# Performance work log

Measured on AMD Instinct MI355X. Metric: run time of the kernel, lower is better.

The kernel has to match this reference:

```python
import jax, jax.numpy as jnp
from jax import lax
import numpy as np

H = 256      # encoder_hidden
F = 256      # variance predictor filter_size
K = 3        # kernel_size
NBINS = 256  # variance_embedding n_bins
B, S, T = 64, 512, 2048


def conv1d(x, w, b, pad):
    # x: [B, L, Cin], w: [K, Cin, Cout] -> [B, L, Cout]
    y = lax.conv_general_dilated(x, w, window_strides=(1,), padding=[(pad, pad)],
                                 dimension_numbers=('NWC', 'WIO', 'NWC'))
    return y + b


def layer_norm(x, g, b, eps=1e-5):
    mu = jnp.mean(x, -1, keepdims=True)
    v = jnp.mean((x - mu) ** 2, -1, keepdims=True)
    return (x - mu) * lax.rsqrt(v + eps) * g + b


def predictor(x, mask, w1, b1, g1, be1, w2, b2, g2, be2, lw, lb):
    h = jax.nn.relu(conv1d(x, w1, b1, (K - 1) // 2))
    h = layer_norm(h, g1, be1)
    h = jax.nn.relu(conv1d(h, w2, b2, 1))  # padding=1 hardcoded in original conv1d_2
    h = layer_norm(h, g2, be2)
    out = (h @ lw + lb)[..., 0]            # [B, L]
    return jnp.where(mask, 0.0, out)       # masked_fill(mask, 0.0)


def setup_inputs():
    key = jax.random.key(0)
    ks = jax.random.split(key, 16)
    inp = {
        'x': jax.random.normal(ks[0], (B, S, H), jnp.float32),
        'pitch_target': jax.random.normal(ks[1], (B, S), jnp.float32),
        'energy_target': jax.random.normal(ks[2], (B, S), jnp.float32),
        'src_mask': jnp.zeros((B, S), bool),
        'duration': jax.random.randint(ks[3], (B, S), 0, 4, jnp.int32),
        'max_len': T,
    }
    i = 4
    for p in ['d', 'p', 'e']:
        inp[p + '_w1'] = jax.random.normal(ks[i], (K, H, F), jnp.float32) * 0.05; i += 1
        inp[p + '_b1'] = jnp.zeros((F,), jnp.float32)
        inp[p + '_g1'] = jnp.ones((F,), jnp.float32)
        inp[p + '_be1'] = jnp.zeros((F,), jnp.float32)
        inp[p + '_w2'] = jax.random.normal(ks[i], (K, F, F), jnp.float32) * 0.05; i += 1
        inp[p + '_b2'] = jnp.zeros((F,), jnp.float32)
        inp[p + '_g2'] = jnp.ones((F,), jnp.float32)
        inp[p + '_be2'] = jnp.zeros((F,), jnp.float32)
        inp[p + '_lw'] = jax.random.normal(ks[i], (F, 1), jnp.float32) * 0.05; i += 1
        inp[p + '_lb'] = jnp.zeros((1,), jnp.float32)
    inp['p_table'] = jax.random.normal(ks[i], (NBINS, H), jnp.float32) * 0.02; i += 1
    inp['e_table'] = jax.random.normal(ks[i], (NBINS, H), jnp.float32) * 0.02
    return inp


def reference(x, pitch_target, energy_target, src_mask, duration, max_len,
              d_w1, d_b1, d_g1, d_be1, d_w2, d_b2, d_g2, d_be2, d_lw, d_lb,
              p_w1, p_b1, p_g1, p_be1, p_w2, p_b2, p_g2, p_be2, p_lw, p_lb,
              e_w1, e_b1, e_g1, e_be1, e_w2, e_b2, e_g2, e_be2, e_lw, e_lb,
              p_table, e_table):
    # linear-quantized bins over the data range (stats.json min/max -> [-2, 2] for randn data)
    bins = jnp.linspace(-2.0, 2.0, NBINS - 1, dtype=jnp.float32)

    log_d_pred = predictor(x, src_mask, d_w1, d_b1, d_g1, d_be1, d_w2, d_b2, d_g2, d_be2, d_lw, d_lb)

    # phoneme-level pitch (training path: target given -> embed bucketized target)
    p_pred = predictor(x, src_mask, p_w1, p_b1, p_g1, p_be1, p_w2, p_b2, p_g2, p_be2, p_lw, p_lb)
    p_emb = p_table[jnp.searchsorted(bins, pitch_target, side='left')]  # torch.bucketize(right=False)
    x = x + p_emb

    # phoneme-level energy (predictor runs on x AFTER pitch embedding, as in original)
    e_pred = predictor(x, src_mask, e_w1, e_b1, e_g1, e_be1, e_w2, e_b2, e_g2, e_be2, e_lw, e_lb)
    e_emb = e_table[jnp.searchsorted(bins, energy_target, side='left')]
    x = x + e_emb

    # Length regulation: expand phoneme i duration[b, i] times, pad to max_len.
    cum = jnp.cumsum(duration, axis=1)                 # [B, S]
    mel_len = cum[:, -1]                               # [B]
    frames = jnp.arange(max_len)                       # [T]
    # frame t maps to first phoneme i with cum[i] > t
    idx = jax.vmap(lambda c: jnp.searchsorted(c, frames, side='right'))(cum)  # [B, T]
    idx = jnp.minimum(idx, duration.shape[1] - 1)
    mel = jnp.take_along_axis(x, idx[:, :, None], axis=1)                     # [B, T, H]
    valid = frames[None, :] < mel_len[:, None]
    mel = jnp.where(valid[:, :, None], mel, 0.0)       # zero-pad beyond mel_len

    d_rounded = duration
    return (mel, p_pred, e_pred, log_d_pred, d_rounded, mel_len)
```

## Files before the change

### kernel.cpp

```cpp
#include <hip/hip_runtime.h>
#include <cstdint>
#include <cstddef>


#define HH 256
#define SS 512
#define BB 64
#define TT 2048
#define LSTR 264

typedef __bf16 bf16;
typedef __attribute__((ext_vector_type(8))) __bf16 bf16x8;
typedef __attribute__((ext_vector_type(4))) __bf16 bf16x4;
typedef __attribute__((ext_vector_type(4))) float f32x4;

static constexpr size_t WSZ  = (size_t)3 * HH * HH;
static constexpr size_t H1SZ = (size_t)BB * SS * HH;

__device__ __forceinline__ float edge_val(int j) {
    const float step = 4.0f / 254.0f;
    if (j == 254) return 2.0f;
    return __fadd_rn(-2.0f, __fmul_rn((float)j, step));
}
__device__ __forceinline__ int bucket256(float v) {
    int lo = 0, hi = 255;
    while (lo < hi) {
        int mid = (lo + hi) >> 1;
        if (edge_val(mid) < v) lo = mid + 1; else hi = mid;
    }
    return lo;
}

__global__ __launch_bounds__(256) void prep_kernel(
    const float* __restrict__ w0, const float* __restrict__ w1,
    const float* __restrict__ w2, const float* __restrict__ w3,
    const float* __restrict__ w4, const float* __restrict__ w5,
    bf16* __restrict__ wp,
    const int* __restrict__ dur, int* __restrict__ idxb, int* __restrict__ mli,
    float* __restrict__ drnd, float* __restrict__ mlen,
    const float* __restrict__ x, const float* __restrict__ pt,
    const float* __restrict__ ptab,
    bf16* __restrict__ x1, bf16* __restrict__ x2)
{
    const int tid = threadIdx.x;
    if (blockIdx.x < 18) {
        const int cv = blockIdx.x / 3, k = blockIdx.x % 3;
        const float* wsel[6] = {w0, w1, w2, w3, w4, w5};
        const float* wk = wsel[cv] + (size_t)k * HH * HH;
        bf16* o = wp + ((size_t)(cv * 3 + k)) * HH * HH;
        for (int fb = 0; fb < 16; ++fb) {
            #pragma unroll
            for (int h = 0; h < 2; ++h) {
                const int idx  = tid + 256 * h;
                const int kcb  = idx >> 6, lane = idx & 63;
                const int f    = fb * 16 + (lane & 15);
                const int c0   = kcb * 32 + (lane >> 4) * 8;
                bf16x8 v;
                #pragma unroll
                for (int j = 0; j < 8; ++j) v[j] = (bf16)wk[(size_t)(c0 + j) * HH + f];
                *(bf16x8*)(o + (((size_t)fb * 8 + kcb) * 64 + lane) * 8) = v;
            }
        }
    } else if (blockIdx.x < 82) {
        __shared__ int sb[SS];
        const int b = blockIdx.x - 18;
        const int d0 = dur[b * SS + tid];
        const int d1 = dur[b * SS + tid + 256];
        drnd[b * SS + tid]       = (float)d0;
        drnd[b * SS + tid + 256] = (float)d1;
        sb[tid]       = d0;
        sb[tid + 256] = d1;
        __syncthreads();
        for (int off = 1; off < SS; off <<= 1) {
            const int a0 = (tid >= off) ? sb[tid - off] : 0;
            const int a1 = (tid + 256 >= off) ? sb[tid + 256 - off] : 0;
            __syncthreads();
            sb[tid] += a0;
            sb[tid + 256] += a1;
            __syncthreads();
        }
        {
            const int hi = sb[tid], lo = hi - d0;
            for (int j = lo; j < hi; ++j) idxb[b * TT + j] = tid;
        }
        {
            const int hi = sb[tid + 256], lo = hi - d1;
            for (int j = lo; j < hi; ++j) idxb[b * TT + j] = tid + 256;
        }
        if (tid == 255) { mlen[b] = (float)sb[SS - 1]; mli[b] = sb[SS - 1]; }
    } else {
        const int row = (blockIdx.x - 82) * 8 + (tid >> 5);
        const int c   = (tid & 31) * 8;
        const int pb  = bucket256(pt[row]);
        const float4 v0 = *(const float4*)(x + (size_t)row * HH + c);
        const float4 v1 = *(const float4*)(x + (size_t)row * HH + c + 4);
        const float4 t0 = *(const float4*)(ptab + (size_t)pb * HH + c);
        const float4 t1 = *(const float4*)(ptab + (size_t)pb * HH + c + 4);
        bf16x8 a, b2;
        a[0] = (bf16)v0.x; a[1] = (bf16)v0.y; a[2] = (bf16)v0.z; a[3] = (bf16)v0.w;
        a[4] = (bf16)v1.x; a[5] = (bf16)v1.y; a[6] = (bf16)v1.z; a[7] = (bf16)v1.w;
        b2[0] = (bf16)(v0.x + t0.x); b2[1] = (bf16)(v0.y + t0.y);
        b2[2] = (bf16)(v0.z + t0.z); b2[3] = (bf16)(v0.w + t0.w);
        b2[4] = (bf16)(v1.x + t1.x); b2[5] = (bf16)(v1.y + t1.y);
        b2[6] = (bf16)(v1.z + t1.z); b2[7] = (bf16)(v1.w + t1.w);
        *(bf16x8*)(x1 + (size_t)row * HH + c) = a;
        *(bf16x8*)(x2 + (size_t)row * HH + c) = b2;
    }
}

struct Args3 {
    const float* bias[3];
    const float* g[3];
    const float* be[3];
    const float* lw[3];
    const float* lb[3];
    float*       out[3];
};

__global__ __launch_bounds__(256, 3) void conv_fused(
    const bf16* __restrict__ x1,
    const bf16* __restrict__ x2,
    const bf16* __restrict__ wpk,
    Args3 a1, Args3 a2,
    const uint8_t* __restrict__ mask)
{
    __shared__ alignas(16) bf16 tile[82 * LSTR];
    __shared__ float red_s[80][4], red_q[80][4];
    __shared__ float ln_m[80], ln_r[80];

    const int tid    = threadIdx.x;
    const int pred   = blockIdx.x >> 9;
    const int within = blockIdx.x & 511;
    const int b      = within >> 3;
    const int s0     = (within & 7) * 64;

    const int lane = tid & 63;
    const int wv   = tid >> 6;

    const bf16* inb = (pred == 2 ? x2 : x1) + (size_t)b * SS * HH;
    const bf16* wt1 = wpk + (size_t)(pred * 2) * WSZ;
    const bf16* wt2 = wt1 + WSZ;

    for (int idx = tid; idx < 82 * 32; idx += 256) {
        const int r   = idx >> 5, c16 = idx & 31;
        const int s   = s0 - 9 + r;
        bf16x8 v = {};
        if (s >= 0 && s < SS)
            v = *(const bf16x8*)(inb + (size_t)s * HH + c16 * 8);
        *(bf16x8*)&tile[r * LSTR + c16 * 8] = v;
    }
    __syncthreads();

    const int ln15 = lane & 15;
    const int g8   = (lane >> 4) << 3;
    const int q4   = (lane >> 4) << 2;

    f32x4 bini[4];
    #pragma unroll
    for (int mf = 0; mf < 4; ++mf)
        #pragma unroll
        for (int i = 0; i < 4; ++i)
            bini[mf][i] = a1.bias[pred][64 * wv + 16 * mf + q4 + i];

    f32x4 acc1[4][5];
    #pragma unroll
    for (int mf = 0; mf < 4; ++mf)
        #pragma unroll
        for (int sf = 0; sf < 5; ++sf) acc1[mf][sf] = bini[mf];

    #pragma unroll 2
    for (int t = 0; t < 24; ++t) {
        const int k = t >> 3, kcb = t & 7;
        const int kc = kcb << 5;
        bf16x8 aw[4], bx[5];
        const bf16* bp = wt1 + ((((size_t)k * 16 + wv * 4) * 8 + kcb) << 9)
                       + (size_t)lane * 8;
        #pragma unroll
        for (int mf = 0; mf < 4; ++mf)
            aw[mf] = *(const bf16x8*)(bp + ((size_t)mf << 12));
        #pragma unroll
        for (int sf = 0; sf < 5; ++sf)
            bx[sf] = *(const bf16x8*)&tile[(16 * sf + ln15 + k) * LSTR + kc + g8];
        __builtin_amdgcn_s_setprio(1);
        #pragma unroll
        for (int mf = 0; mf < 4; ++mf)
            #pragma unroll
            for (int sf = 0; sf < 5; ++sf)
                acc1[mf][sf] = __builtin_amdgcn_mfma_f32_16x16x32_bf16(
                    aw[mf], bx[sf], acc1[mf][sf], 0, 0, 0);
        __builtin_amdgcn_s_setprio(0);
    }

    bf16x8 aw20[4];
    {
        const bf16* bp2 = wt2 + (((size_t)wv * 4) * 8 << 9) + (size_t)lane * 8;
        #pragma unroll
        for (int mf = 0; mf < 4; ++mf)
            aw20[mf] = *(const bf16x8*)(bp2 + ((size_t)mf << 12));
    }

    #pragma unroll
    for (int mf = 0; mf < 4; ++mf)
        #pragma unroll
        for (int sf = 0; sf < 5; ++sf)
            #pragma unroll
            for (int i = 0; i < 4; ++i)
                acc1[mf][sf][i] = fmaxf(acc1[mf][sf][i], 0.f);

    #pragma unroll
    for (int sf = 0; sf < 5; ++sf) {
        float s = 0.f, q = 0.f;
        #pragma unroll
        for (int mf = 0; mf < 4; ++mf)
            #pragma unroll
            for (int i = 0; i < 4; ++i) {
                const float v = acc1[mf][sf][i];
                s += v; q += v * v;
            }
        s += __shfl_xor(s, 16); s += __shfl_xor(s, 32);
        q += __shfl_xor(q, 16); q += __shfl_xor(q, 32);
        if (lane < 16) { red_s[16 * sf + lane][wv] = s; red_q[16 * sf + lane][wv] = q; }
    }
    __syncthreads();
    if (tid < 80) {
        const float s = red_s[tid][0] + red_s[tid][1] + red_s[tid][2] + red_s[tid][3];
        const float q = red_q[tid][0] + red_q[tid][1] + red_q[tid][2] + red_q[tid][3];
        const float mean = s * (1.f / 256.f);
        const float var  = q * (1.f / 256.f) - mean * mean;
        ln_m[tid] = mean;
        ln_r[tid] = rsqrtf(var + 1e-5f);
    }
    __syncthreads();

    {
        float g1v[4][4], be1v[4][4];
        #pragma unroll
        for (int mf = 0; mf < 4; ++mf)
            #pragma unroll
            for (int i = 0; i < 4; ++i) {
                const int f1 = 64 * wv + 16 * mf + q4 + i;
                g1v[mf][i]  = a1.g[pred][f1];
                be1v[mf][i] = a1.be[pred][f1];
            }
        #pragma unroll
        for (int sf = 0; sf < 5; ++sf) {
            const int o  = 16 * sf + ln15;
            const int hr = o - 7;
            const float mean = ln_m[o], rs = ln_r[o];
            const bool ok = (o >= 7 && o <= 72);
            #pragma unroll
            for (int mf = 0; mf < 4; ++mf) {
                bf16x4 hv;
                #pragma unroll
                for (int i = 0; i < 4; ++i)
                    hv[i] = (bf16)((acc1[mf][sf][i] - mean) * rs * g1v[mf][i] + be1v[mf][i]);
                if (ok)
                    *(bf16x4*)&tile[hr * LSTR + 64 * wv + 16 * mf + q4] = hv;
            }
        }
    }
    __syncthreads();
    if (tid < 64) {
        if (s0 == 0)       *(uint2*)&tile[tid * 4]            = make_uint2(0u, 0u);
        if (s0 == SS - 64) *(uint2*)&tile[65 * LSTR + tid * 4] = make_uint2(0u, 0u);
    }
    __syncthreads();

    #pragma unroll
    for (int mf = 0; mf < 4; ++mf)
        #pragma unroll
        for (int i = 0; i < 4; ++i)
            bini[mf][i] = a2.bias[pred][64 * wv + 16 * mf + q4 + i];

    f32x4 acc2[4][4];
    #pragma unroll
    for (int mf = 0; mf < 4; ++mf)
        #pragma unroll
        for (int sf = 0; sf < 4; ++sf) acc2[mf][sf] = bini[mf];

#define S2_STEP(AW_, K_, KCB_) do {                                            \
    const int kc_ = (KCB_) << 5;                                               \
    bf16x8 bx_[4];                                                             \
    _Pragma("unroll")                                                          \
    for (int sf_ = 0; sf_ < 4; ++sf_)                                          \
        bx_[sf_] = *(const bf16x8*)&tile[(16 * sf_ + ln15 + (K_)) * LSTR       \
                                         + kc_ + g8];                          \
    __builtin_amdgcn_s_setprio(1);                                             \
    _Pragma("unroll")                                                          \
    for (int mf_ = 0; mf_ < 4; ++mf_)                                          \
        _Pragma("unroll")                                                      \
        for (int sf_ = 0; sf_ < 4; ++sf_)                                      \
            acc2[mf_][sf_] = __builtin_amdgcn_mfma_f32_16x16x32_bf16(          \
                AW_[mf_], bx_[sf_], acc2[mf_][sf_], 0, 0, 0);                  \
    __builtin_amdgcn_s_setprio(0);                                             \
} while (0)

    S2_STEP(aw20, 0, 0);
    #pragma unroll 2
    for (int t = 1; t < 24; ++t) {
        const int k = t >> 3, kcb = t & 7;
        bf16x8 aw[4];
        const bf16* bp = wt2 + ((((size_t)k * 16 + wv * 4) * 8 + kcb) << 9)
                       + (size_t)lane * 8;
        #pragma unroll
        for (int mf = 0; mf < 4; ++mf)
            aw[mf] = *(const bf16x8*)(bp + ((size_t)mf << 12));
        S2_STEP(aw, k, kcb);
    }
#undef S2_STEP

    #pragma unroll
    for (int mf = 0; mf < 4; ++mf)
        #pragma unroll
        for (int sf = 0; sf < 4; ++sf)
            #pragma unroll
            for (int i = 0; i < 4; ++i)
                acc2[mf][sf][i] = fmaxf(acc2[mf][sf][i], 0.f);

    #pragma unroll
    for (int sf = 0; sf < 4; ++sf) {
        float s = 0.f, q = 0.f;
        #pragma unroll
        for (int mf = 0; mf < 4; ++mf)
            #pragma unroll
            for (int i = 0; i < 4; ++i) {
                const float v = acc2[mf][sf][i];
                s += v; q += v * v;
            }
        s += __shfl_xor(s, 16); s += __shfl_xor(s, 32);
        q += __shfl_xor(q, 16); q += __shfl_xor(q, 32);
        if (lane < 16) { red_s[16 * sf + lane][wv] = s; red_q[16 * sf + lane][wv] = q; }
    }
    __syncthreads();
    if (tid < 64) {
        const float s = red_s[tid][0] + red_s[tid][1] + red_s[tid][2] + red_s[tid][3];
        const float q = red_q[tid][0] + red_q[tid][1] + red_q[tid][2] + red_q[tid][3];
        const float mean = s * (1.f / 256.f);
        const float var  = q * (1.f / 256.f) - mean * mean;
        ln_m[tid] = mean;
        ln_r[tid] = rsqrtf(var + 1e-5f);
    }
    __syncthreads();

    {
        float c1v[4][4], cbv[4][4];
        #pragma unroll
        for (int mf = 0; mf < 4; ++mf)
            #pragma unroll
            for (int i = 0; i < 4; ++i) {
                const int f2 = 64 * wv + 16 * mf + q4 + i;
                const float lwv = a2.lw[pred][f2];
                c1v[mf][i] = a2.g[pred][f2] * lwv;
                cbv[mf][i] = a2.be[pred][f2] * lwv;
            }
        #pragma unroll
        for (int sf = 0; sf < 4; ++sf) {
            const int so = 16 * sf + ln15;
            const float mean = ln_m[so], rs = ln_r[so];
            float t = 0.f;
            #pragma unroll
            for (int mf = 0; mf < 4; ++mf)
                #pragma unroll
                for (int i = 0; i < 4; ++i)
                    t += (acc2[mf][sf][i] - mean) * rs * c1v[mf][i] + cbv[mf][i];
            t += __shfl_xor(t, 16); t += __shfl_xor(t, 32);
            if (lane < 16) red_s[16 * sf + lane][wv] = t;
        }
        __syncthreads();
        if (tid < 64) {
            const int gr = b * SS + s0 + tid;
            const float dv = red_s[tid][0] + red_s[tid][1] + red_s[tid][2] + red_s[tid][3]
                           + a2.lb[pred][0];
            a2.out[pred][gr] = mask[gr] ? 0.f : dv;
        }
    }
}

__global__ __launch_bounds__(256) void gather_kernel(
    const float* __restrict__ x,
    const float* __restrict__ ptab, const float* __restrict__ pt,
    const float* __restrict__ etab, const float* __restrict__ et,
    const int* __restrict__ idxb, const int* __restrict__ mli,
    float* __restrict__ mel)
{
    const int lane = threadIdx.x & 63;
    for (int row = blockIdx.x * 4 + (threadIdx.x >> 6); row < BB * TT; row += 4096 * 4) {
        const int b = row >> 11;
        const int t = row & (TT - 1);
        float4 v = make_float4(0.f, 0.f, 0.f, 0.f);
        if (t < mli[b]) {
            const int idx = idxb[row];
            const size_t src = ((size_t)b * SS + idx) * HH + lane * 4;
            v = *(const float4*)(x + src);
            const int pb = bucket256(pt[b * SS + idx]);
            const int eb = bucket256(et[b * SS + idx]);
            const float4 pv = *(const float4*)(ptab + (size_t)pb * HH + lane * 4);
            const float4 ev = *(const float4*)(etab + (size_t)eb * HH + lane * 4);
            v.x += pv.x + ev.x; v.y += pv.y + ev.y; v.z += pv.z + ev.z; v.w += pv.w + ev.w;
        }
        *(float4*)(mel + (size_t)row * HH + lane * 4) = v;
    }
}

extern "C" void kernel_launch(void* const* d_in, const int* in_sizes, int n_in,
                              void* d_out, int out_size, void* d_ws, size_t ws_size,
                              hipStream_t stream) {
    (void)in_sizes; (void)n_in; (void)out_size; (void)ws_size;

    const float*   x      = (const float*)d_in[0];
    const float*   pitch  = (const float*)d_in[1];
    const float*   energy = (const float*)d_in[2];
    const uint8_t* mask   = (const uint8_t*)d_in[3];
    const int*     dur    = (const int*)d_in[4];
    const float*   ptab   = (const float*)d_in[36];
    const float*   etab   = (const float*)d_in[37];

    float* out = (float*)d_out;
    const size_t N_MEL = (size_t)BB * TT * HH;
    float* out_p  = out + N_MEL;
    float* out_e  = out_p + (size_t)BB * SS;
    float* out_ld = out_e + (size_t)BB * SS;
    float* out_dr = out_ld + (size_t)BB * SS;
    float* out_ml = out_dr + (size_t)BB * SS;

    bf16* wpk  = (bf16*)d_ws;
    int*  idxb = (int*)(wpk + 6 * WSZ);
    int*  mli  = idxb + (size_t)BB * TT;

    bf16* x1 = (bf16*)out;
    bf16* x2 = x1 + H1SZ;

    prep_kernel<<<18 + 64 + 4096, 256, 0, stream>>>(
        (const float*)d_in[6],  (const float*)d_in[10],
        (const float*)d_in[16], (const float*)d_in[20],
        (const float*)d_in[26], (const float*)d_in[30],
        wpk,
        dur, idxb, mli, out_dr, out_ml,
        x, pitch, ptab, x1, x2);

    Args3 a1 = {
        {(const float*)d_in[7],  (const float*)d_in[17], (const float*)d_in[27]},
        {(const float*)d_in[8],  (const float*)d_in[18], (const float*)d_in[28]},
        {(const float*)d_in[9],  (const float*)d_in[19], (const float*)d_in[29]},
        {nullptr, nullptr, nullptr}, {nullptr, nullptr, nullptr},
        {nullptr, nullptr, nullptr}
    };
    Args3 a2 = {
        {(const float*)d_in[11], (const float*)d_in[21], (const float*)d_in[31]},
        {(const float*)d_in[12], (const float*)d_in[22], (const float*)d_in[32]},
        {(const float*)d_in[13], (const float*)d_in[23], (const float*)d_in[33]},
        {(const float*)d_in[14], (const float*)d_in[24], (const float*)d_in[34]},
        {(const float*)d_in[15], (const float*)d_in[25], (const float*)d_in[35]},
        {out_ld, out_p, out_e}
    };

    conv_fused<<<3 * 512, 256, 0, stream>>>(x1, x2, wpk, a1, a2, mask);

    gather_kernel<<<4096, 256, 0, stream>>>(x, ptab, pitch, etab, energy, idxb, mli, out);
}
```

Before: 132.2 us.

## Fuse bf16 input staging and mel gather into a single mega kernel

Removes the separate bf16 copies of x and x+pitch-embedding that the prep kernel used to write. The conv blocks now load fp32 x directly, add the pitch embedding on the fly for the energy predictor, and convert to bf16 in shared memory. The mel gather kernel is merged into the same launch as extra blocks, so gather work can overlap with the conv blocks and one launch disappears. The cost is redundant fp32 reads of halo rows and table lookups per conv block, plus gather blocks competing with conv blocks for occupancy and sharing the conv kernel's shared-memory and register footprint.

```diff
diff --git a/kernel.cpp b/kernel.cpp
--- a/kernel.cpp
+++ b/kernel.cpp
@@ -14,8 +14,7 @@
 typedef __attribute__((ext_vector_type(4))) __bf16 bf16x4;
 typedef __attribute__((ext_vector_type(4))) float f32x4;
 
-static constexpr size_t WSZ  = (size_t)3 * HH * HH;
-static constexpr size_t H1SZ = (size_t)BB * SS * HH;
+static constexpr size_t WSZ = (size_t)3 * HH * HH;
 
 __device__ __forceinline__ float edge_val(int j) {
     const float step = 4.0f / 254.0f;
@@ -37,10 +36,7 @@
     const float* __restrict__ w4, const float* __restrict__ w5,
     bf16* __restrict__ wp,
     const int* __restrict__ dur, int* __restrict__ idxb, int* __restrict__ mli,
-    float* __restrict__ drnd, float* __restrict__ mlen,
-    const float* __restrict__ x, const float* __restrict__ pt,
-    const float* __restrict__ ptab,
-    bf16* __restrict__ x1, bf16* __restrict__ x2)
+    float* __restrict__ drnd, float* __restrict__ mlen)
 {
     const int tid = threadIdx.x;
     if (blockIdx.x < 18) {
@@ -61,7 +57,7 @@
                 *(bf16x8*)(o + (((size_t)fb * 8 + kcb) * 64 + lane) * 8) = v;
             }
         }
-    } else if (blockIdx.x < 82) {
+    } else {
         __shared__ int sb[SS];
         const int b = blockIdx.x - 18;
         const int d0 = dur[b * SS + tid];
@@ -88,23 +84,6 @@
             for (int j = lo; j < hi; ++j) idxb[b * TT + j] = tid + 256;
         }
         if (tid == 255) { mlen[b] = (float)sb[SS - 1]; mli[b] = sb[SS - 1]; }
-    } else {
-        const int row = (blockIdx.x - 82) * 8 + (tid >> 5);
-        const int c   = (tid & 31) * 8;
-        const int pb  = bucket256(pt[row]);
-        const float4 v0 = *(const float4*)(x + (size_t)row * HH + c);
-        const float4 v1 = *(const float4*)(x + (size_t)row * HH + c + 4);
-        const float4 t0 = *(const float4*)(ptab + (size_t)pb * HH + c);
-        const float4 t1 = *(const float4*)(ptab + (size_t)pb * HH + c + 4);
-        bf16x8 a, b2;
-        a[0] = (bf16)v0.x; a[1] = (bf16)v0.y; a[2] = (bf16)v0.z; a[3] = (bf16)v0.w;
-        a[4] = (bf16)v1.x; a[5] = (bf16)v1.y; a[6] = (bf16)v1.z; a[7] = (bf16)v1.w;
-        b2[0] = (bf16)(v0.x + t0.x); b2[1] = (bf16)(v0.y + t0.y);
-        b2[2] = (bf16)(v0.z + t0.z); b2[3] = (bf16)(v0.w + t0.w);
-        b2[4] = (bf16)(v1.x + t1.x); b2[5] = (bf16)(v1.y + t1.y);
-        b2[6] = (bf16)(v1.z + t1.z); b2[7] = (bf16)(v1.w + t1.w);
-        *(bf16x8*)(x1 + (size_t)row * HH + c) = a;
-        *(bf16x8*)(x2 + (size_t)row * HH + c) = b2;
     }
 }
 
@@ -117,37 +96,81 @@
     float*       out[3];
 };
 
-__global__ __launch_bounds__(256, 3) void conv_fused(
-    const bf16* __restrict__ x1,
-    const bf16* __restrict__ x2,
+__global__ __launch_bounds__(256, 3) void mega_kernel(
+    const float* __restrict__ x,
+    const float* __restrict__ pt,
+    const float* __restrict__ et,
+    const float* __restrict__ ptab, const float* __restrict__ etab,
     const bf16* __restrict__ wpk,
     Args3 a1, Args3 a2,
-    const uint8_t* __restrict__ mask)
+    const uint8_t* __restrict__ mask,
+    const int* __restrict__ idxb, const int* __restrict__ mli,
+    float* __restrict__ mel)
 {
+    const int tid = threadIdx.x;
+
+    if (blockIdx.x >= 1536) {
+        const int lane = tid & 63;
+        for (int row = (blockIdx.x - 1536) * 4 + (tid >> 6); row < BB * TT;
+             row += 4096 * 4) {
+            const int b = row >> 11;
+            const int t = row & (TT - 1);
+            float4 v = make_float4(0.f, 0.f, 0.f, 0.f);
+            if (t < mli[b]) {
+                const int idx = idxb[row];
+                const size_t src = ((size_t)b * SS + idx) * HH + lane * 4;
+                v = *(const float4*)(x + src);
+                const int pb = bucket256(pt[b * SS + idx]);
+                const int eb = bucket256(et[b * SS + idx]);
+                const float4 pv = *(const float4*)(ptab + (size_t)pb * HH + lane * 4);
+                const float4 ev = *(const float4*)(etab + (size_t)eb * HH + lane * 4);
+                v.x += pv.x + ev.x; v.y += pv.y + ev.y;
+                v.z += pv.z + ev.z; v.w += pv.w + ev.w;
+            }
+            *(float4*)(mel + (size_t)row * HH + lane * 4) = v;
+        }
+        return;
+    }
+
     __shared__ alignas(16) bf16 tile[82 * LSTR];
     __shared__ float red_s[80][4], red_q[80][4];
     __shared__ float ln_m[80], ln_r[80];
-
-    const int tid    = threadIdx.x;
+    __shared__ int remb[82];
+
     const int pred   = blockIdx.x >> 9;
     const int within = blockIdx.x & 511;
     const int b      = within >> 3;
     const int s0     = (within & 7) * 64;
+    const bool emb   = (pred == 2);
 
     const int lane = tid & 63;
     const int wv   = tid >> 6;
 
-    const bf16* inb = (pred == 2 ? x2 : x1) + (size_t)b * SS * HH;
+    const float* xb  = x + (size_t)b * SS * HH;
     const bf16* wt1 = wpk + (size_t)(pred * 2) * WSZ;
     const bf16* wt2 = wt1 + WSZ;
 
-    for (int idx = tid; idx < 82 * 32; idx += 256) {
-        const int r   = idx >> 5, c16 = idx & 31;
-        const int s   = s0 - 9 + r;
-        bf16x8 v = {};
-        if (s >= 0 && s < SS)
-            v = *(const bf16x8*)(inb + (size_t)s * HH + c16 * 8);
-        *(bf16x8*)&tile[r * LSTR + c16 * 8] = v;
+    if (emb) {
+        if (tid < 82) {
+            const int s = s0 - 9 + tid;
+            remb[tid] = (s >= 0 && s < SS) ? bucket256(pt[b * SS + s]) : 0;
+        }
+        __syncthreads();
+    }
+
+    for (int idx = tid; idx < 82 * 64; idx += 256) {
+        const int r  = idx >> 6, c4 = (idx & 63) << 2;
+        const int s  = s0 - 9 + r;
+        float4 v = make_float4(0.f, 0.f, 0.f, 0.f);
+        if (s >= 0 && s < SS) {
+            v = *(const float4*)(xb + (size_t)s * HH + c4);
+            if (emb) {
+                const float4 tv = *(const float4*)(ptab + (size_t)remb[r] * HH + c4);
+                v.x += tv.x; v.y += tv.y; v.z += tv.z; v.w += tv.w;
+            }
+        }
+        bf16x4 bv = {(bf16)v.x, (bf16)v.y, (bf16)v.z, (bf16)v.w};
+        *(bf16x4*)&tile[r * LSTR + c4] = bv;
     }
     __syncthreads();
 
@@ -376,32 +399,6 @@
     }
 }
 
-__global__ __launch_bounds__(256) void gather_kernel(
-    const float* __restrict__ x,
-    const float* __restrict__ ptab, const float* __restrict__ pt,
-    const float* __restrict__ etab, const float* __restrict__ et,
-    const int* __restrict__ idxb, const int* __restrict__ mli,
-    float* __restrict__ mel)
-{
-    const int lane = threadIdx.x & 63;
-    for (int row = blockIdx.x * 4 + (threadIdx.x >> 6); row < BB * TT; row += 4096 * 4) {
-        const int b = row >> 11;
-        const int t = row & (TT - 1);
-        float4 v = make_float4(0.f, 0.f, 0.f, 0.f);
-        if (t < mli[b]) {
-            const int idx = idxb[row];
-            const size_t src = ((size_t)b * SS + idx) * HH + lane * 4;
-            v = *(const float4*)(x + src);
-            const int pb = bucket256(pt[b * SS + idx]);
-            const int eb = bucket256(et[b * SS + idx]);
-            const float4 pv = *(const float4*)(ptab + (size_t)pb * HH + lane * 4);
-            const float4 ev = *(const float4*)(etab + (size_t)eb * HH + lane * 4);
-            v.x += pv.x + ev.x; v.y += pv.y + ev.y; v.z += pv.z + ev.z; v.w += pv.w + ev.w;
-        }
-        *(float4*)(mel + (size_t)row * HH + lane * 4) = v;
-    }
-}
-
 extern "C" void kernel_launch(void* const* d_in, const int* in_sizes, int n_in,
                               void* d_out, int out_size, void* d_ws, size_t ws_size,
                               hipStream_t stream) {
@@ -427,16 +424,12 @@
     int*  idxb = (int*)(wpk + 6 * WSZ);
     int*  mli  = idxb + (size_t)BB * TT;
 
-    bf16* x1 = (bf16*)out;
-    bf16* x2 = x1 + H1SZ;
-
-    prep_kernel<<<18 + 64 + 4096, 256, 0, stream>>>(
+    prep_kernel<<<18 + 64, 256, 0, stream>>>(
         (const float*)d_in[6],  (const float*)d_in[10],
         (const float*)d_in[16], (const float*)d_in[20],
         (const float*)d_in[26], (const float*)d_in[30],
         wpk,
-        dur, idxb, mli, out_dr, out_ml,
-        x, pitch, ptab, x1, x2);
+        dur, idxb, mli, out_dr, out_ml);
 
     Args3 a1 = {
         {(const float*)d_in[7],  (const float*)d_in[17], (const float*)d_in[27]},
@@ -454,7 +447,6 @@
         {out_ld, out_p, out_e}
     };
 
-    conv_fused<<<3 * 512, 256, 0, stream>>>(x1, x2, wpk, a1, a2, mask);
-
-    gather_kernel<<<4096, 256, 0, stream>>>(x, ptab, pitch, etab, energy, idxb, mli, out);
+    mega_kernel<<<1536 + 4096, 256, 0, stream>>>(
+        x, pitch, energy, ptab, etab, wpk, a1, a2, mask, idxb, mli, out);
 }
```

After: 146.6 us. +10.9%, slower.
